# Performance work log

Measured on AMD Instinct MI355X. Metric: run time of the kernel, lower is better.

Reference implementation:

```python
import jax, jax.numpy as jnp
import numpy as np

N_NODES = 50000
N_EDGES = 600000
IN_DIM, HID_DIM, OUT_DIM = 128, 256, 40


def setup_inputs() -> dict:
    key = jax.random.key(0)
    ks = jax.random.split(key, 10)
    x = jax.random.normal(ks[0], (N_NODES, IN_DIM), dtype=jnp.float32)
    edge_index = jax.random.randint(ks[1], (2, N_EDGES), 0, N_NODES, dtype=jnp.int64)
    def lin(k, out_d, in_d):
        s = 1.0 / np.sqrt(in_d)
        return jax.random.uniform(k, (out_d, in_d), jnp.float32, -s, s)
    # SAGEConv: lin_l (on aggregated neighbors, with bias) + lin_r (on self, no bias)
    params = {
        "Wl1": lin(ks[2], HID_DIM, IN_DIM), "bl1": jnp.zeros((HID_DIM,), jnp.float32), "Wr1": lin(ks[3], HID_DIM, IN_DIM),
        "Wl2": lin(ks[4], HID_DIM, HID_DIM), "bl2": jnp.zeros((HID_DIM,), jnp.float32), "Wr2": lin(ks[5], HID_DIM, HID_DIM),
        "Wl3": lin(ks[6], OUT_DIM, HID_DIM), "bl3": jnp.zeros((OUT_DIM,), jnp.float32), "Wr3": lin(ks[7], OUT_DIM, HID_DIM),
    }
    return {"x": x, "edge_index": edge_index, **params}


def _sage_conv(x, src, dst, Wl, bl, Wr):
    # mean-aggregate source features into destination nodes
    n = x.shape[0]
    agg = jax.ops.segment_sum(x[src], dst, num_segments=n)          # [N, d_in]
    cnt = jax.ops.segment_sum(jnp.ones_like(dst, dtype=x.dtype), dst, num_segments=n)
    mean = agg / jnp.maximum(cnt, 1.0)[:, None]
    return mean @ Wl.T + bl + x @ Wr.T


def reference(x, edge_index, Wl1, bl1, Wr1, Wl2, bl2, Wr2, Wl3, bl3, Wr3):
    src, dst = edge_index[0], edge_index[1]
    h = _sage_conv(x, src, dst, Wl1, bl1, Wr1)
    h = jax.nn.relu(h)  # dropout is identity in eval mode
    h = _sage_conv(h, src, dst, Wl2, bl2, Wr2)
    h = jax.nn.relu(h)
    h = _sage_conv(h, src, dst, Wl3, bl3, Wr3)
    return jax.nn.log_softmax(h, axis=1)
```

## Files before the change

### kernel.cpp

```cpp
#include <hip/hip_runtime.h>
#include <hip/hip_bf16.h>

#define IN_DIM 128
#define HID_DIM 256
#define OUT_DIM 40
#define SCAN_CHUNK 2048

typedef __attribute__((ext_vector_type(8))) __bf16 bf16x8;
typedef __attribute__((ext_vector_type(4))) float f32x4;

__device__ inline ushort f2bf(float f) {
    uint u = __builtin_bit_cast(uint, f);
    u = (u + 0x7fff + ((u >> 16) & 1)) >> 16;
    return (ushort)u;
}
__device__ inline float bfl(uint u) { return __builtin_bit_cast(float, u << 16); }
__device__ inline float bfh(uint u) { return __builtin_bit_cast(float, u & 0xffff0000u); }

__global__ __launch_bounds__(256) void cvt_x(const float* __restrict__ in,
                                             ushort* __restrict__ out, int n4) {
    int i = blockIdx.x * 256 + threadIdx.x;
    if (i < n4) {
        float4 v = ((const float4*)in)[i];
        uint2 o;
        o.x = (uint)f2bf(v.x) | ((uint)f2bf(v.y) << 16);
        o.y = (uint)f2bf(v.z) | ((uint)f2bf(v.w) << 16);
        ((uint2*)out)[i] = o;
    }
}

__global__ __launch_bounds__(256) void cvt_weights(
    const float* __restrict__ Wl1, const float* __restrict__ Wr1,
    const float* __restrict__ Wl2, const float* __restrict__ Wr2,
    const float* __restrict__ Wl3, const float* __restrict__ Wr3,
    ushort* __restrict__ o1l, ushort* __restrict__ o1r,
    ushort* __restrict__ o2l, ushort* __restrict__ o2r,
    ushort* __restrict__ o3l, ushort* __restrict__ o3r) {
    int idx = blockIdx.x * 256 + threadIdx.x;
    if (idx < 32768) {
        o1l[idx] = f2bf(Wl1[idx]);
        o1r[idx] = f2bf(Wr1[idx]);
        return;
    }
    idx -= 32768;
    if (idx < 65536) {
        o2l[idx] = f2bf(Wl2[idx]);
        o2r[idx] = f2bf(Wr2[idx]);
        return;
    }
    idx -= 65536;
    if (idx < 48 * 256) {
        int row = idx >> 8;
        int col = idx & 255;
        ushort vl = 0, vr = 0;
        if (row < OUT_DIM) {
            vl = f2bf(Wl3[row * 256 + col]);
            vr = f2bf(Wr3[row * 256 + col]);
        }
        o3l[idx] = vl;
        o3r[idx] = vr;
    }
}

__global__ __launch_bounds__(256) void hist_kernel(const int* __restrict__ dst,
                                                   int* __restrict__ cnt, int E) {
    int e = blockIdx.x * 256 + threadIdx.x;
    if (e < E) atomicAdd(&cnt[dst[e]], 1);
}

__global__ __launch_bounds__(256) void scan_pass1(const int* __restrict__ cnt,
                                                  int* __restrict__ bsum, int N) {
    __shared__ int red[256];
    const int base = blockIdx.x * SCAN_CHUNK;
    int s = 0;
    for (int i = threadIdx.x; i < SCAN_CHUNK; i += 256) {
        int idx = base + i;
        if (idx < N) s += cnt[idx];
    }
    red[threadIdx.x] = s;
    __syncthreads();
    for (int o = 128; o > 0; o >>= 1) {
        if (threadIdx.x < o) red[threadIdx.x] += red[threadIdx.x + o];
        __syncthreads();
    }
    if (threadIdx.x == 0) bsum[blockIdx.x] = red[0];
}

__global__ __launch_bounds__(256) void scan_pass3(const int* __restrict__ cnt,
                                                  const int* __restrict__ bsum,
                                                  int* __restrict__ rowptr,
                                                  int* __restrict__ cursor,
                                                  float* __restrict__ inv,
                                                  int N, int E, int SB) {
    __shared__ int ls[256];
    __shared__ int boff;
    if (threadIdx.x == 0) {
        int r = 0;
        for (int i = 0; i < blockIdx.x; ++i) r += bsum[i];
        boff = r;
    }
    const int tbase = blockIdx.x * SCAN_CHUNK + threadIdx.x * 8;
    int c[8];
    int s = 0;
#pragma unroll
    for (int j = 0; j < 8; ++j) {
        int idx = tbase + j;
        c[j] = (idx < N) ? cnt[idx] : 0;
        s += c[j];
    }
    ls[threadIdx.x] = s;
    __syncthreads();
    for (int o = 1; o < 256; o <<= 1) {
        int u = (threadIdx.x >= o) ? ls[threadIdx.x - o] : 0;
        __syncthreads();
        ls[threadIdx.x] += u;
        __syncthreads();
    }
    int run = boff + ls[threadIdx.x] - s;
#pragma unroll
    for (int j = 0; j < 8; ++j) {
        int idx = tbase + j;
        if (idx < N) {
            rowptr[idx] = run;
            cursor[idx] = run;
            inv[idx] = 1.0f / fmaxf((float)c[j], 1.0f);
            run += c[j];
        }
    }
    if (blockIdx.x == 0 && threadIdx.x == 0) rowptr[N] = E;
}

__global__ __launch_bounds__(256) void fill_kernel(const int* __restrict__ src,
                                                   const int* __restrict__ dst,
                                                   int* __restrict__ cursor,
                                                   int* __restrict__ srcs, int E) {
    int e = blockIdx.x * 256 + threadIdx.x;
    if (e < E) {
        int pos = atomicAdd(&cursor[dst[e]], 1);
        srcs[pos] = src[e];
    }
}

template <int D>
__global__ __launch_bounds__(256) void gather_mean_bf(const ushort* __restrict__ feat,
                                                      const int* __restrict__ rowptr,
                                                      const int* __restrict__ srcs,
                                                      const float* __restrict__ inv,
                                                      ushort* __restrict__ out, int N) {
    constexpr int V = D / 64;
    const int wave = threadIdx.x >> 6;
    const int lane = threadIdx.x & 63;
    const int n = blockIdx.x * 4 + wave;
    if (n >= N) return;
    const int beg = rowptr[n];
    const int end = rowptr[n + 1];
    const int col = lane * V;
    float a0 = 0.f, a1 = 0.f, a2 = 0.f, a3 = 0.f;
    int e = beg;
    if constexpr (V == 4) {
        for (; e + 7 < end; e += 8) {
            uint2 q[8];
#pragma unroll
            for (int j = 0; j < 8; ++j)
                q[j] = *(const uint2*)&feat[(long long)srcs[e + j] * D + col];
#pragma unroll
            for (int j = 0; j < 8; ++j) {
                a0 += bfl(q[j].x); a1 += bfh(q[j].x);
                a2 += bfl(q[j].y); a3 += bfh(q[j].y);
            }
        }
        for (; e + 3 < end; e += 4) {
            uint2 q[4];
#pragma unroll
            for (int j = 0; j < 4; ++j)
                q[j] = *(const uint2*)&feat[(long long)srcs[e + j] * D + col];
#pragma unroll
            for (int j = 0; j < 4; ++j) {
                a0 += bfl(q[j].x); a1 += bfh(q[j].x);
                a2 += bfl(q[j].y); a3 += bfh(q[j].y);
            }
        }
        for (; e < end; ++e) {
            uint2 q0 = *(const uint2*)&feat[(long long)srcs[e] * D + col];
            a0 += bfl(q0.x); a1 += bfh(q0.x); a2 += bfl(q0.y); a3 += bfh(q0.y);
        }
        const float sc = inv[n];
        uint2 o;
        o.x = (uint)f2bf(a0 * sc) | ((uint)f2bf(a1 * sc) << 16);
        o.y = (uint)f2bf(a2 * sc) | ((uint)f2bf(a3 * sc) << 16);
        *(uint2*)&out[(long long)n * D + col] = o;
    } else {
        for (; e + 7 < end; e += 8) {
            uint q[8];
#pragma unroll
            for (int j = 0; j < 8; ++j)
                q[j] = *(const uint*)&feat[(long long)srcs[e + j] * D + col];
#pragma unroll
            for (int j = 0; j < 8; ++j) {
                a0 += bfl(q[j]); a1 += bfh(q[j]);
            }
        }
        for (; e + 3 < end; e += 4) {
            uint q[4];
#pragma unroll
            for (int j = 0; j < 4; ++j)
                q[j] = *(const uint*)&feat[(long long)srcs[e + j] * D + col];
#pragma unroll
            for (int j = 0; j < 4; ++j) {
                a0 += bfl(q[j]); a1 += bfh(q[j]);
            }
        }
        for (; e < end; ++e) {
            uint q0 = *(const uint*)&feat[(long long)srcs[e] * D + col];
            a0 += bfl(q0); a1 += bfh(q0);
        }
        const float sc = inv[n];
        uint o = (uint)f2bf(a0 * sc) | ((uint)f2bf(a1 * sc) << 16);
        *(uint*)&out[(long long)n * D + col] = o;
    }
}

template <int K, bool RELU, bool OUTBF>
__global__ __launch_bounds__(256, 3) void sage_gemm_mfma(const ushort* __restrict__ Amean,
                                                         const ushort* __restrict__ Aself,
                                                         const ushort* __restrict__ Wl,
                                                         const float* __restrict__ bias,
                                                         const ushort* __restrict__ Wr,
                                                         void* __restrict__ outv, int N, int O) {
    constexpr int KP = K + 8;
    constexpr int NK = K / 32;
    __shared__ __align__(16) ushort Ws[64 * KP];

    const int tid = threadIdx.x;
    const int wave = tid >> 6;
    const int lane = tid & 63;
    const int ln = lane & 15;
    const int quad = lane >> 4;
    const int bm0 = blockIdx.y * 128;
    const int bn0 = blockIdx.x * 64;

    int arow[2];
#pragma unroll
    for (int rt = 0; rt < 2; ++rt) {
        int r = bm0 + wave * 32 + rt * 16 + ln;
        arow[rt] = min(r, N - 1);
    }

    f32x4 acc[2][4] = {};

    for (int phase = 0; phase < 2; ++phase) {
        const ushort* __restrict__ A = phase ? Aself : Amean;
        const ushort* __restrict__ W = phase ? Wr : Wl;

        __syncthreads();
#pragma unroll
        for (int i = tid; i < 64 * (K / 8); i += 256) {
            int row = i / (K / 8);
            int c8 = (i % (K / 8)) * 8;
            *(ulonglong2*)&Ws[row * KP + c8] =
                *(const ulonglong2*)&W[(long long)(bn0 + row) * K + c8];
        }
        __syncthreads();

        bf16x8 areg[NK][2];
#pragma unroll
        for (int kk = 0; kk < NK; ++kk)
#pragma unroll
            for (int rt = 0; rt < 2; ++rt)
                areg[kk][rt] = *(const bf16x8*)&A[(long long)arow[rt] * K + kk * 32 + quad * 8];

#pragma unroll
        for (int kk = 0; kk < NK; ++kk) {
#pragma unroll
            for (int ct = 0; ct < 4; ++ct) {
                bf16x8 b = *(const bf16x8*)&Ws[(ct * 16 + ln) * KP + kk * 32 + quad * 8];
#pragma unroll
                for (int rt = 0; rt < 2; ++rt)
                    acc[rt][ct] = __builtin_amdgcn_mfma_f32_16x16x32_bf16(areg[kk][rt], b, acc[rt][ct], 0, 0, 0);
            }
        }
    }

#pragma unroll
    for (int rt = 0; rt < 2; ++rt) {
        int rbase = bm0 + wave * 32 + rt * 16 + quad * 4;
#pragma unroll
        for (int ct = 0; ct < 4; ++ct) {
            int col = bn0 + ct * 16 + ln;
            if (col >= O) continue;
            float bv = bias[col];
#pragma unroll
            for (int r = 0; r < 4; ++r) {
                int row = rbase + r;
                if (row >= N) continue;
                float v = acc[rt][ct][r] + bv;
                if (RELU) v = fmaxf(v, 0.f);
                if (OUTBF)
                    ((ushort*)outv)[(long long)row * O + col] = f2bf(v);
                else
                    ((float*)outv)[(long long)row * O + col] = v;
            }
        }
    }
}

template <int K>
__global__ __launch_bounds__(256, 3) void sage_gemm_pre(const ushort* __restrict__ A0,
                                                        const ushort* __restrict__ Wl,
                                                        const ushort* __restrict__ Wr,
                                                        ushort* __restrict__ P,
                                                        float* __restrict__ S, int N, int O) {
    constexpr int KP = 2 * K + 8;
    constexpr int NK = K / 32;
    __shared__ __align__(16) ushort Ws[48 * KP];

    const int tid = threadIdx.x;
    const int wave = tid >> 6;
    const int lane = tid & 63;
    const int ln = lane & 15;
    const int quad = lane >> 4;
    const int bm0 = blockIdx.x * 64;

    const int arow = min(bm0 + wave * 16 + ln, N - 1);

#pragma unroll
    for (int i = tid; i < 48 * (K / 8); i += 256) {
        int row = i / (K / 8);
        int c8 = (i % (K / 8)) * 8;
        *(ulonglong2*)&Ws[row * KP + c8] =
            *(const ulonglong2*)&Wl[(long long)row * K + c8];
        *(ulonglong2*)&Ws[row * KP + K + c8] =
            *(const ulonglong2*)&Wr[(long long)row * K + c8];
    }
    __syncthreads();

#pragma unroll
    for (int phase = 0; phase < 2; ++phase) {
        f32x4 acc[3] = {};
#pragma unroll
        for (int kk = 0; kk < NK; ++kk) {
            bf16x8 a = *(const bf16x8*)&A0[(long long)arow * K + kk * 32 + quad * 8];
#pragma unroll
            for (int ct = 0; ct < 3; ++ct) {
                bf16x8 b = *(const bf16x8*)&Ws[(ct * 16 + ln) * KP + phase * K + kk * 32 + quad * 8];
                acc[ct] = __builtin_amdgcn_mfma_f32_16x16x32_bf16(a, b, acc[ct], 0, 0, 0);
            }
        }
        int rbase = bm0 + wave * 16 + quad * 4;
#pragma unroll
        for (int ct = 0; ct < 3; ++ct) {
            int col = ct * 16 + ln;
            if (col >= O) continue;
#pragma unroll
            for (int r = 0; r < 4; ++r) {
                int row = rbase + r;
                if (row >= N) continue;
                if (phase == 0)
                    P[(long long)row * O + col] = f2bf(acc[ct][r]);
                else
                    S[(long long)row * O + col] = acc[ct][r];
            }
        }
    }
}

__global__ __launch_bounds__(256) void agg_bias_lsm(const ushort* __restrict__ P,
                                                    const float* __restrict__ S,
                                                    const float* __restrict__ bias,
                                                    const int* __restrict__ rowptr,
                                                    const int* __restrict__ srcs,
                                                    const float* __restrict__ inv,
                                                    float* __restrict__ out, int N) {
    const int wave = threadIdx.x >> 6;
    const int lane = threadIdx.x & 63;
    const int n = blockIdx.x * 4 + wave;
    if (n >= N) return;
    const int beg = rowptr[n];
    const int end = rowptr[n + 1];
    const bool act = lane < OUT_DIM;
    const int cidx = act ? lane : 0;

    float acc = 0.f;
    int e = beg;
    for (; e + 3 < end; e += 4) {
        int s0 = srcs[e], s1 = srcs[e + 1], s2 = srcs[e + 2], s3 = srcs[e + 3];
        float v0 = __builtin_bit_cast(float, (uint)P[(long long)s0 * OUT_DIM + cidx] << 16);
        float v1 = __builtin_bit_cast(float, (uint)P[(long long)s1 * OUT_DIM + cidx] << 16);
        float v2 = __builtin_bit_cast(float, (uint)P[(long long)s2 * OUT_DIM + cidx] << 16);
        float v3 = __builtin_bit_cast(float, (uint)P[(long long)s3 * OUT_DIM + cidx] << 16);
        acc += (v0 + v1) + (v2 + v3);
    }
    for (; e < end; ++e)
        acc += __builtin_bit_cast(float, (uint)P[(long long)srcs[e] * OUT_DIM + cidx] << 16);

    float v = act ? (acc * inv[n] + S[(long long)n * OUT_DIM + lane] + bias[lane]) : -INFINITY;
    float m = v;
#pragma unroll
    for (int o = 32; o > 0; o >>= 1) m = fmaxf(m, __shfl_xor(m, o, 64));
    float ex = act ? expf(v - m) : 0.f;
    float sm = ex;
#pragma unroll
    for (int o = 32; o > 0; o >>= 1) sm += __shfl_xor(sm, o, 64);
    float ls = logf(sm);
    if (act) out[(long long)n * OUT_DIM + lane] = v - m - ls;
}

extern "C" void kernel_launch(void* const* d_in, const int* in_sizes, int n_in,
                              void* d_out, int out_size, void* d_ws, size_t ws_size,
                              hipStream_t stream) {
    const float* x   = (const float*)d_in[0];
    const int*   ei  = (const int*)d_in[1];
    const float* Wl1 = (const float*)d_in[2];
    const float* bl1 = (const float*)d_in[3];
    const float* Wr1 = (const float*)d_in[4];
    const float* Wl2 = (const float*)d_in[5];
    const float* bl2 = (const float*)d_in[6];
    const float* Wr2 = (const float*)d_in[7];
    const float* Wl3 = (const float*)d_in[8];
    const float* bl3 = (const float*)d_in[9];
    const float* Wr3 = (const float*)d_in[10];
    float* out = (float*)d_out;

    const int N = in_sizes[0] / IN_DIM;
    const int E = in_sizes[1] / 2;
    const int* src = ei;
    const int* dst = ei + E;

    char* w = (char*)d_ws;
    size_t off = 0;
    auto alloc = [&](size_t bytes) {
        void* p = w + off;
        off = (off + bytes + 255) & ~(size_t)255;
        return p;
    };
    ushort* xb   = (ushort*)alloc((size_t)N * IN_DIM * 2);
    ushort* M    = (ushort*)alloc((size_t)N * HID_DIM * 2);
    ushort* H1   = (ushort*)alloc((size_t)N * HID_DIM * 2);
    ushort* H2   = (ushort*)alloc((size_t)N * HID_DIM * 2);
    ushort* P3   = (ushort*)alloc((size_t)N * OUT_DIM * 2);
    float*  S3   = (float*)alloc((size_t)N * OUT_DIM * 4);
    float*  inv  = (float*)alloc((size_t)N * 4);
    int*    cnt  = (int*)alloc((size_t)N * 4);
    int*    rowptr = (int*)alloc((size_t)(N + 1) * 4);
    int*    cursor = (int*)alloc((size_t)N * 4);
    int*    srcs = (int*)alloc((size_t)E * 4);
    int*    bsum = (int*)alloc(256 * 4);
    ushort* Wl1b = (ushort*)alloc(256 * 128 * 2);
    ushort* Wr1b = (ushort*)alloc(256 * 128 * 2);
    ushort* Wl2b = (ushort*)alloc(256 * 256 * 2);
    ushort* Wr2b = (ushort*)alloc(256 * 256 * 2);
    ushort* Wl3b = (ushort*)alloc(48 * 256 * 2);
    ushort* Wr3b = (ushort*)alloc(48 * 256 * 2);

    cvt_x<<<(N * IN_DIM / 4 + 255) / 256, 256, 0, stream>>>(x, xb, N * IN_DIM / 4);
    cvt_weights<<<(32768 + 65536 + 48 * 256 + 255) / 256, 256, 0, stream>>>(
        Wl1, Wr1, Wl2, Wr2, Wl3, Wr3, Wl1b, Wr1b, Wl2b, Wr2b, Wl3b, Wr3b);

    const int SB = (N + SCAN_CHUNK - 1) / SCAN_CHUNK;
    hipMemsetAsync(cnt, 0, (size_t)N * sizeof(int), stream);
    hist_kernel<<<(E + 255) / 256, 256, 0, stream>>>(dst, cnt, E);
    scan_pass1<<<SB, 256, 0, stream>>>(cnt, bsum, N);
    scan_pass3<<<SB, 256, 0, stream>>>(cnt, bsum, rowptr, cursor, inv, N, E, SB);
    fill_kernel<<<(E + 255) / 256, 256, 0, stream>>>(src, dst, cursor, srcs, E);

    const int gm = (N + 127) / 128;
    const int gg = (N + 3) / 4;

    gather_mean_bf<IN_DIM><<<gg, 256, 0, stream>>>(xb, rowptr, srcs, inv, M, N);
    sage_gemm_mfma<IN_DIM, true, true><<<dim3(4, gm), 256, 0, stream>>>(
        M, xb, Wl1b, bl1, Wr1b, H1, N, HID_DIM);

    gather_mean_bf<HID_DIM><<<gg, 256, 0, stream>>>(H1, rowptr, srcs, inv, M, N);
    sage_gemm_mfma<HID_DIM, true, true><<<dim3(4, gm), 256, 0, stream>>>(
        M, H1, Wl2b, bl2, Wr2b, H2, N, HID_DIM);

    sage_gemm_pre<HID_DIM><<<(N + 63) / 64, 256, 0, stream>>>(
        H2, Wl3b, Wr3b, P3, S3, N, OUT_DIM);
    agg_bias_lsm<<<gg, 256, 0, stream>>>(P3, S3, bl3, rowptr, srcs, inv, out, N);
}
```

Measured before the change: 357.7 us.

## Rewrite SAGE GEMM to stage A and W tiles via global_load_lds DMA

Replaces the layer 1/2 GEMM with a version that loads 128x32 tiles of both the activation and weight matrices straight into LDS using global_load_lds, iterating over K steps for both the mean and self halves. The block tile grows from 128x64 to 128x128 with a 2x2 wave layout (64x64 per wave), halving the grid's column dimension and raising MFMA reuse per loaded fragment. The old path loaded all of A into registers and all of W into LDS per phase. The new loop has two barriers per 32-wide K step and no double buffering, so load latency may be exposed. The accumulator footprint per wave is larger, which may cut occupancy.

Result: no change. 360.7 us (+0.8%).

```diff
diff --git a/kernel.cpp b/kernel.cpp
--- a/kernel.cpp
+++ b/kernel.cpp
@@ -8,6 +8,12 @@
 
 typedef __attribute__((ext_vector_type(8))) __bf16 bf16x8;
 typedef __attribute__((ext_vector_type(4))) float f32x4;
+typedef __attribute__((address_space(1))) void gvoid;
+typedef __attribute__((address_space(3))) void lvoid;
+
+__device__ __forceinline__ void gl16(const void* g, void* l) {
+    __builtin_amdgcn_global_load_lds((gvoid*)g, (lvoid*)l, 16, 0, 0);
+}
 
 __device__ inline ushort f2bf(float f) {
     uint u = __builtin_bit_cast(uint, f);
@@ -220,16 +226,16 @@
     }
 }
 
-template <int K, bool RELU, bool OUTBF>
-__global__ __launch_bounds__(256, 3) void sage_gemm_mfma(const ushort* __restrict__ Amean,
-                                                         const ushort* __restrict__ Aself,
-                                                         const ushort* __restrict__ Wl,
-                                                         const float* __restrict__ bias,
-                                                         const ushort* __restrict__ Wr,
-                                                         void* __restrict__ outv, int N, int O) {
-    constexpr int KP = K + 8;
-    constexpr int NK = K / 32;
-    __shared__ __align__(16) ushort Ws[64 * KP];
+template <int K, bool RELU>
+__global__ __launch_bounds__(256, 3) void sage_gemm_dma(const ushort* __restrict__ Amean,
+                                                        const ushort* __restrict__ Aself,
+                                                        const ushort* __restrict__ Wl,
+                                                        const float* __restrict__ bias,
+                                                        const ushort* __restrict__ Wr,
+                                                        ushort* __restrict__ outp, int N, int O) {
+    constexpr int NSTEP = 2 * K / 32;
+    __shared__ __align__(16) char As[8192];
+    __shared__ __align__(16) char Bs[8192];
 
     const int tid = threadIdx.x;
     const int wave = tid >> 6;
@@ -237,56 +243,56 @@
     const int ln = lane & 15;
     const int quad = lane >> 4;
     const int bm0 = blockIdx.y * 128;
-    const int bn0 = blockIdx.x * 64;
-
-    int arow[2];
-#pragma unroll
-    for (int rt = 0; rt < 2; ++rt) {
-        int r = bm0 + wave * 32 + rt * 16 + ln;
-        arow[rt] = min(r, N - 1);
-    }
-
-    f32x4 acc[2][4] = {};
-
-    for (int phase = 0; phase < 2; ++phase) {
-        const ushort* __restrict__ A = phase ? Aself : Amean;
-        const ushort* __restrict__ W = phase ? Wr : Wl;
+    const int bn0 = blockIdx.x * 128;
+    const int rh = (wave >> 1) * 64;
+    const int ch = (wave & 1) * 64;
+
+    const int c0 = wave * 2, c1 = wave * 2 + 1;
+    const int o0 = c0 * 1024 + lane * 16;
+    const int o1 = c1 * 1024 + lane * 16;
+    const int q0 = o0 >> 11, r0 = (o0 >> 4) & 127;
+    const int q1 = o1 >> 11, r1 = (o1 >> 4) & 127;
+    const long long ar0 = min(bm0 + r0, N - 1);
+    const long long ar1 = min(bm0 + r1, N - 1);
+    const long long wr0 = bn0 + r0;
+    const long long wr1 = bn0 + r1;
+
+    f32x4 acc[4][4] = {};
+
+#pragma unroll
+    for (int s = 0; s < NSTEP; ++s) {
+        const int kk = s * 32;
+        const ushort* __restrict__ A = (kk < K) ? Amean : Aself;
+        const ushort* __restrict__ W = (kk < K) ? Wl : Wr;
+        const int kp = kk & (K - 1);
 
         __syncthreads();
-#pragma unroll
-        for (int i = tid; i < 64 * (K / 8); i += 256) {
-            int row = i / (K / 8);
-            int c8 = (i % (K / 8)) * 8;
-            *(ulonglong2*)&Ws[row * KP + c8] =
-                *(const ulonglong2*)&W[(long long)(bn0 + row) * K + c8];
-        }
+        gl16(&A[ar0 * K + kp + q0 * 8], As + c0 * 1024);
+        gl16(&A[ar1 * K + kp + q1 * 8], As + c1 * 1024);
+        gl16(&W[wr0 * K + kp + q0 * 8], Bs + c0 * 1024);
+        gl16(&W[wr1 * K + kp + q1 * 8], Bs + c1 * 1024);
         __syncthreads();
 
-        bf16x8 areg[NK][2];
-#pragma unroll
-        for (int kk = 0; kk < NK; ++kk)
-#pragma unroll
-            for (int rt = 0; rt < 2; ++rt)
-                areg[kk][rt] = *(const bf16x8*)&A[(long long)arow[rt] * K + kk * 32 + quad * 8];
-
-#pragma unroll
-        for (int kk = 0; kk < NK; ++kk) {
-#pragma unroll
-            for (int ct = 0; ct < 4; ++ct) {
-                bf16x8 b = *(const bf16x8*)&Ws[(ct * 16 + ln) * KP + kk * 32 + quad * 8];
-#pragma unroll
-                for (int rt = 0; rt < 2; ++rt)
-                    acc[rt][ct] = __builtin_amdgcn_mfma_f32_16x16x32_bf16(areg[kk][rt], b, acc[rt][ct], 0, 0, 0);
-            }
-        }
-    }
-
-#pragma unroll
-    for (int rt = 0; rt < 2; ++rt) {
-        int rbase = bm0 + wave * 32 + rt * 16 + quad * 4;
+        bf16x8 a[4], b[4];
+#pragma unroll
+        for (int rt = 0; rt < 4; ++rt)
+            a[rt] = *(const bf16x8*)(As + quad * 2048 + (rh + rt * 16 + ln) * 16);
+#pragma unroll
+        for (int ct = 0; ct < 4; ++ct)
+            b[ct] = *(const bf16x8*)(Bs + quad * 2048 + (ch + ct * 16 + ln) * 16);
+#pragma unroll
+        for (int rt = 0; rt < 4; ++rt)
+#pragma unroll
+            for (int ct = 0; ct < 4; ++ct)
+                acc[rt][ct] = __builtin_amdgcn_mfma_f32_16x16x32_bf16(a[rt], b[ct], acc[rt][ct], 0, 0, 0);
+    }
+
+#pragma unroll
+    for (int rt = 0; rt < 4; ++rt) {
+        int rbase = bm0 + rh + rt * 16 + quad * 4;
 #pragma unroll
         for (int ct = 0; ct < 4; ++ct) {
-            int col = bn0 + ct * 16 + ln;
+            int col = bn0 + ch + ct * 16 + ln;
             if (col >= O) continue;
             float bv = bias[col];
 #pragma unroll
@@ -295,10 +301,7 @@
                 if (row >= N) continue;
                 float v = acc[rt][ct][r] + bv;
                 if (RELU) v = fmaxf(v, 0.f);
-                if (OUTBF)
-                    ((ushort*)outv)[(long long)row * O + col] = f2bf(v);
-                else
-                    ((float*)outv)[(long long)row * O + col] = v;
+                outp[(long long)row * O + col] = f2bf(v);
             }
         }
     }
@@ -467,11 +470,11 @@
     const int gg = (N + 3) / 4;
 
     gather_mean_bf<IN_DIM><<<gg, 256, 0, stream>>>(xb, rowptr, srcs, inv, M, N);
-    sage_gemm_mfma<IN_DIM, true, true><<<dim3(4, gm), 256, 0, stream>>>(
+    sage_gemm_dma<IN_DIM, true><<<dim3(2, gm), 256, 0, stream>>>(
         M, xb, Wl1b, bl1, Wr1b, H1, N, HID_DIM);
 
     gather_mean_bf<HID_DIM><<<gg, 256, 0, stream>>>(H1, rowptr, srcs, inv, M, N);
-    sage_gemm_mfma<HID_DIM, true, true><<<dim3(4, gm), 256, 0, stream>>>(
+    sage_gemm_dma<HID_DIM, true><<<dim3(2, gm), 256, 0, stream>>>(
         M, H1, Wl2b, bl2, Wr2b, H2, N, HID_DIM);
 
     sage_gemm_pre<HID_DIM><<<(N + 63) / 64, 256, 0, stream>>>(
```

## Fuse neighbor mean-gather into SAGE GEMM via shared-memory tile

Applied to the files above, without the earlier changes.

Replaces the separate gather_mean kernel and MFMA GEMM for layers 1 and 2 with one fused kernel. Each block gathers the mean-aggregated features of 64 nodes into LDS, then loops over all output column tiles, reloading Wl and Wr into LDS for each. This removes the global write and re-read of the intermediate mean matrix and one launch per layer. In exchange each block restages all weights, runs serial per-wave node gathers (16 nodes per wave) with less parallelism, and uses more LDS, which lowers occupancy.

Result: slower. 415.1 us (+16.0%).

```diff
diff --git a/kernel.cpp b/kernel.cpp
--- a/kernel.cpp
+++ b/kernel.cpp
@@ -141,94 +141,16 @@
     }
 }
 
-template <int D>
-__global__ __launch_bounds__(256) void gather_mean_bf(const ushort* __restrict__ feat,
-                                                      const int* __restrict__ rowptr,
-                                                      const int* __restrict__ srcs,
-                                                      const float* __restrict__ inv,
-                                                      ushort* __restrict__ out, int N) {
-    constexpr int V = D / 64;
-    const int wave = threadIdx.x >> 6;
-    const int lane = threadIdx.x & 63;
-    const int n = blockIdx.x * 4 + wave;
-    if (n >= N) return;
-    const int beg = rowptr[n];
-    const int end = rowptr[n + 1];
-    const int col = lane * V;
-    float a0 = 0.f, a1 = 0.f, a2 = 0.f, a3 = 0.f;
-    int e = beg;
-    if constexpr (V == 4) {
-        for (; e + 7 < end; e += 8) {
-            uint2 q[8];
-#pragma unroll
-            for (int j = 0; j < 8; ++j)
-                q[j] = *(const uint2*)&feat[(long long)srcs[e + j] * D + col];
-#pragma unroll
-            for (int j = 0; j < 8; ++j) {
-                a0 += bfl(q[j].x); a1 += bfh(q[j].x);
-                a2 += bfl(q[j].y); a3 += bfh(q[j].y);
-            }
-        }
-        for (; e + 3 < end; e += 4) {
-            uint2 q[4];
-#pragma unroll
-            for (int j = 0; j < 4; ++j)
-                q[j] = *(const uint2*)&feat[(long long)srcs[e + j] * D + col];
-#pragma unroll
-            for (int j = 0; j < 4; ++j) {
-                a0 += bfl(q[j].x); a1 += bfh(q[j].x);
-                a2 += bfl(q[j].y); a3 += bfh(q[j].y);
-            }
-        }
-        for (; e < end; ++e) {
-            uint2 q0 = *(const uint2*)&feat[(long long)srcs[e] * D + col];
-            a0 += bfl(q0.x); a1 += bfh(q0.x); a2 += bfl(q0.y); a3 += bfh(q0.y);
-        }
-        const float sc = inv[n];
-        uint2 o;
-        o.x = (uint)f2bf(a0 * sc) | ((uint)f2bf(a1 * sc) << 16);
-        o.y = (uint)f2bf(a2 * sc) | ((uint)f2bf(a3 * sc) << 16);
-        *(uint2*)&out[(long long)n * D + col] = o;
-    } else {
-        for (; e + 7 < end; e += 8) {
-            uint q[8];
-#pragma unroll
-            for (int j = 0; j < 8; ++j)
-                q[j] = *(const uint*)&feat[(long long)srcs[e + j] * D + col];
-#pragma unroll
-            for (int j = 0; j < 8; ++j) {
-                a0 += bfl(q[j]); a1 += bfh(q[j]);
-            }
-        }
-        for (; e + 3 < end; e += 4) {
-            uint q[4];
-#pragma unroll
-            for (int j = 0; j < 4; ++j)
-                q[j] = *(const uint*)&feat[(long long)srcs[e + j] * D + col];
-#pragma unroll
-            for (int j = 0; j < 4; ++j) {
-                a0 += bfl(q[j]); a1 += bfh(q[j]);
-            }
-        }
-        for (; e < end; ++e) {
-            uint q0 = *(const uint*)&feat[(long long)srcs[e] * D + col];
-            a0 += bfl(q0); a1 += bfh(q0);
-        }
-        const float sc = inv[n];
-        uint o = (uint)f2bf(a0 * sc) | ((uint)f2bf(a1 * sc) << 16);
-        *(uint*)&out[(long long)n * D + col] = o;
-    }
-}
-
-template <int K, bool RELU, bool OUTBF>
-__global__ __launch_bounds__(256, 3) void sage_gemm_mfma(const ushort* __restrict__ Amean,
-                                                         const ushort* __restrict__ Aself,
-                                                         const ushort* __restrict__ Wl,
-                                                         const float* __restrict__ bias,
-                                                         const ushort* __restrict__ Wr,
-                                                         void* __restrict__ outv, int N, int O) {
+template <int K, int MINW>
+__global__ __launch_bounds__(256, MINW) void sage_fused(
+    const ushort* __restrict__ feat, const int* __restrict__ rowptr,
+    const int* __restrict__ srcs, const float* __restrict__ inv,
+    const ushort* __restrict__ Wl, const float* __restrict__ bias,
+    const ushort* __restrict__ Wr, ushort* __restrict__ outp, int N) {
     constexpr int KP = K + 8;
     constexpr int NK = K / 32;
+    constexpr int V = K / 64;
+    __shared__ __align__(16) ushort As[64 * KP];
     __shared__ __align__(16) ushort Ws[64 * KP];
 
     const int tid = threadIdx.x;
@@ -236,69 +158,123 @@
     const int lane = tid & 63;
     const int ln = lane & 15;
     const int quad = lane >> 4;
-    const int bm0 = blockIdx.y * 128;
-    const int bn0 = blockIdx.x * 64;
-
-    int arow[2];
-#pragma unroll
-    for (int rt = 0; rt < 2; ++rt) {
-        int r = bm0 + wave * 32 + rt * 16 + ln;
-        arow[rt] = min(r, N - 1);
-    }
-
-    f32x4 acc[2][4] = {};
-
-    for (int phase = 0; phase < 2; ++phase) {
-        const ushort* __restrict__ A = phase ? Aself : Amean;
-        const ushort* __restrict__ W = phase ? Wr : Wl;
-
-        __syncthreads();
-#pragma unroll
-        for (int i = tid; i < 64 * (K / 8); i += 256) {
-            int row = i / (K / 8);
-            int c8 = (i % (K / 8)) * 8;
-            *(ulonglong2*)&Ws[row * KP + c8] =
-                *(const ulonglong2*)&W[(long long)(bn0 + row) * K + c8];
-        }
-        __syncthreads();
-
-        bf16x8 areg[NK][2];
-#pragma unroll
-        for (int kk = 0; kk < NK; ++kk)
-#pragma unroll
-            for (int rt = 0; rt < 2; ++rt)
-                areg[kk][rt] = *(const bf16x8*)&A[(long long)arow[rt] * K + kk * 32 + quad * 8];
-
-#pragma unroll
-        for (int kk = 0; kk < NK; ++kk) {
-#pragma unroll
-            for (int ct = 0; ct < 4; ++ct) {
-                bf16x8 b = *(const bf16x8*)&Ws[(ct * 16 + ln) * KP + kk * 32 + quad * 8];
-#pragma unroll
-                for (int rt = 0; rt < 2; ++rt)
-                    acc[rt][ct] = __builtin_amdgcn_mfma_f32_16x16x32_bf16(areg[kk][rt], b, acc[rt][ct], 0, 0, 0);
-            }
-        }
-    }
-
-#pragma unroll
-    for (int rt = 0; rt < 2; ++rt) {
-        int rbase = bm0 + wave * 32 + rt * 16 + quad * 4;
-#pragma unroll
-        for (int ct = 0; ct < 4; ++ct) {
-            int col = bn0 + ct * 16 + ln;
-            if (col >= O) continue;
+    const int bm0 = blockIdx.x * 64;
+
+    for (int i = 0; i < 16; ++i) {
+        const int n = bm0 + wave * 16 + i;
+        if (n >= N) break;
+        const int beg = rowptr[n];
+        const int end = rowptr[n + 1];
+        const int col = lane * V;
+        float a0 = 0.f, a1 = 0.f, a2 = 0.f, a3 = 0.f;
+        int e = beg;
+        if constexpr (V == 4) {
+            for (; e + 7 < end; e += 8) {
+                uint2 q[8];
+#pragma unroll
+                for (int j = 0; j < 8; ++j)
+                    q[j] = *(const uint2*)&feat[(long long)srcs[e + j] * K + col];
+#pragma unroll
+                for (int j = 0; j < 8; ++j) {
+                    a0 += bfl(q[j].x); a1 += bfh(q[j].x);
+                    a2 += bfl(q[j].y); a3 += bfh(q[j].y);
+                }
+            }
+            for (; e + 3 < end; e += 4) {
+                uint2 q[4];
+#pragma unroll
+                for (int j = 0; j < 4; ++j)
+                    q[j] = *(const uint2*)&feat[(long long)srcs[e + j] * K + col];
+#pragma unroll
+                for (int j = 0; j < 4; ++j) {
+                    a0 += bfl(q[j].x); a1 += bfh(q[j].x);
+                    a2 += bfl(q[j].y); a3 += bfh(q[j].y);
+                }
+            }
+            for (; e < end; ++e) {
+                uint2 q0 = *(const uint2*)&feat[(long long)srcs[e] * K + col];
+                a0 += bfl(q0.x); a1 += bfh(q0.x); a2 += bfl(q0.y); a3 += bfh(q0.y);
+            }
+            const float sc = inv[n];
+            uint2 o;
+            o.x = (uint)f2bf(a0 * sc) | ((uint)f2bf(a1 * sc) << 16);
+            o.y = (uint)f2bf(a2 * sc) | ((uint)f2bf(a3 * sc) << 16);
+            *(uint2*)&As[(wave * 16 + i) * KP + col] = o;
+        } else {
+            for (; e + 7 < end; e += 8) {
+                uint q[8];
+#pragma unroll
+                for (int j = 0; j < 8; ++j)
+                    q[j] = *(const uint*)&feat[(long long)srcs[e + j] * K + col];
+#pragma unroll
+                for (int j = 0; j < 8; ++j) {
+                    a0 += bfl(q[j]); a1 += bfh(q[j]);
+                }
+            }
+            for (; e + 3 < end; e += 4) {
+                uint q[4];
+#pragma unroll
+                for (int j = 0; j < 4; ++j)
+                    q[j] = *(const uint*)&feat[(long long)srcs[e + j] * K + col];
+#pragma unroll
+                for (int j = 0; j < 4; ++j) {
+                    a0 += bfl(q[j]); a1 += bfh(q[j]);
+                }
+            }
+            for (; e < end; ++e) {
+                uint q0 = *(const uint*)&feat[(long long)srcs[e] * K + col];
+                a0 += bfl(q0); a1 += bfh(q0);
+            }
+            const float sc = inv[n];
+            uint o = (uint)f2bf(a0 * sc) | ((uint)f2bf(a1 * sc) << 16);
+            *(uint*)&As[(wave * 16 + i) * KP + col] = o;
+        }
+    }
+
+    const int arow = min(bm0 + wave * 16 + ln, N - 1);
+
+    f32x4 acc[4];
+    for (int ct = 0; ct < 4; ++ct) {
+#pragma unroll
+        for (int ph = 0; ph < 2; ++ph) {
+            const ushort* __restrict__ W = ph ? Wr : Wl;
+            __syncthreads();
+#pragma unroll
+            for (int i = tid; i < 64 * (K / 8); i += 256) {
+                int row = i / (K / 8);
+                int c8 = (i % (K / 8)) * 8;
+                *(ulonglong2*)&Ws[row * KP + c8] =
+                    *(const ulonglong2*)&W[(long long)(ct * 64 + row) * K + c8];
+            }
+            __syncthreads();
+            if (ph == 0) {
+#pragma unroll
+                for (int c4 = 0; c4 < 4; ++c4) acc[c4] = (f32x4){0.f, 0.f, 0.f, 0.f};
+            }
+#pragma unroll
+            for (int kk = 0; kk < NK; ++kk) {
+                bf16x8 a;
+                if (ph == 0)
+                    a = *(const bf16x8*)&As[(wave * 16 + ln) * KP + kk * 32 + quad * 8];
+                else
+                    a = *(const bf16x8*)&feat[(long long)arow * K + kk * 32 + quad * 8];
+#pragma unroll
+                for (int c4 = 0; c4 < 4; ++c4) {
+                    bf16x8 b = *(const bf16x8*)&Ws[(c4 * 16 + ln) * KP + kk * 32 + quad * 8];
+                    acc[c4] = __builtin_amdgcn_mfma_f32_16x16x32_bf16(a, b, acc[c4], 0, 0, 0);
+                }
+            }
+        }
+        int rbase = bm0 + wave * 16 + quad * 4;
+#pragma unroll
+        for (int c4 = 0; c4 < 4; ++c4) {
+            int col = ct * 64 + c4 * 16 + ln;
             float bv = bias[col];
 #pragma unroll
             for (int r = 0; r < 4; ++r) {
                 int row = rbase + r;
-                if (row >= N) continue;
-                float v = acc[rt][ct][r] + bv;
-                if (RELU) v = fmaxf(v, 0.f);
-                if (OUTBF)
-                    ((ushort*)outv)[(long long)row * O + col] = f2bf(v);
-                else
-                    ((float*)outv)[(long long)row * O + col] = v;
+                if (row < N)
+                    outp[(long long)row * HID_DIM + col] = f2bf(fmaxf(acc[c4][r] + bv, 0.f));
             }
         }
     }
@@ -434,7 +410,6 @@
         return p;
     };
     ushort* xb   = (ushort*)alloc((size_t)N * IN_DIM * 2);
-    ushort* M    = (ushort*)alloc((size_t)N * HID_DIM * 2);
     ushort* H1   = (ushort*)alloc((size_t)N * HID_DIM * 2);
     ushort* H2   = (ushort*)alloc((size_t)N * HID_DIM * 2);
     ushort* P3   = (ushort*)alloc((size_t)N * OUT_DIM * 2);
@@ -463,18 +438,16 @@
     scan_pass3<<<SB, 256, 0, stream>>>(cnt, bsum, rowptr, cursor, inv, N, E, SB);
     fill_kernel<<<(E + 255) / 256, 256, 0, stream>>>(src, dst, cursor, srcs, E);
 
-    const int gm = (N + 127) / 128;
+    const int gb = (N + 63) / 64;
     const int gg = (N + 3) / 4;
 
-    gather_mean_bf<IN_DIM><<<gg, 256, 0, stream>>>(xb, rowptr, srcs, inv, M, N);
-    sage_gemm_mfma<IN_DIM, true, true><<<dim3(4, gm), 256, 0, stream>>>(
-        M, xb, Wl1b, bl1, Wr1b, H1, N, HID_DIM);
-
-    gather_mean_bf<HID_DIM><<<gg, 256, 0, stream>>>(H1, rowptr, srcs, inv, M, N);
-    sage_gemm_mfma<HID_DIM, true, true><<<dim3(4, gm), 256, 0, stream>>>(
-        M, H1, Wl2b, bl2, Wr2b, H2, N, HID_DIM);
-
-    sage_gemm_pre<HID_DIM><<<(N + 63) / 64, 256, 0, stream>>>(
+    sage_fused<IN_DIM, 4><<<gb, 256, 0, stream>>>(
+        xb, rowptr, srcs, inv, Wl1b, bl1, Wr1b, H1, N);
+
+    sage_fused<HID_DIM, 2><<<gb, 256, 0, stream>>>(
+        H1, rowptr, srcs, inv, Wl2b, bl2, Wr2b, H2, N);
+
+    sage_gemm_pre<HID_DIM><<<gb, 256, 0, stream>>>(
         H2, Wl3b, Wr3b, P3, S3, N, OUT_DIM);
     agg_bias_lsm<<<gg, 256, 0, stream>>>(P3, S3, bl3, rowptr, srcs, inv, out, N);
 }
```
